# Kernel optimization log

Measured on AMD Instinct MI355X. Metric: run time of the kernel, lower is better.

Reference implementation:

```python
import jax, jax.numpy as jnp
import numpy as np

B, N, C, H, MLP = 4, 1024, 768, 6, 2304  # num_heads = C // 128
D = C // H  # head dim = 128


def setup_inputs() -> dict:
    key = jax.random.key(0)
    ks = iter(jax.random.split(key, 64))
    def nrm(shape, s=0.02):
        return jax.random.normal(next(ks), shape, jnp.float32) * s
    inp = {}
    for nm in ("queries", "change_emb", "imageA_emb", "imageB_emb", "pe"):
        inp[nm] = jax.random.normal(next(ks), (B, N, C), jnp.float32)
    # three Attention modules: self-attn (1), change->ABC cross (2), imageAB->change cross (3)
    for i in (1, 2, 3):
        for p in ("q", "k", "v", "o"):
            inp[f"w{p}{i}"] = nrm((C, C))       # stored [in, out]; y = x @ W + b
            inp[f"b{p}{i}"] = jnp.zeros((C,), jnp.float32)
    for i in (1, 2, 3):
        inp[f"ln{i}_w"] = jnp.ones((C,), jnp.float32)
        inp[f"ln{i}_b"] = jnp.zeros((C,), jnp.float32)
    inp["mlp_w1"] = nrm((C, MLP)); inp["mlp_b1"] = jnp.zeros((MLP,), jnp.float32)
    inp["mlp_w2"] = nrm((MLP, C)); inp["mlp_b2"] = jnp.zeros((C,), jnp.float32)
    inp["flag_a"] = nrm((C,)); inp["flag_b"] = nrm((C,)); inp["flag_c"] = nrm((C,))
    return inp


def _ln(x, w, b, eps=1e-5):
    m = jnp.mean(x, -1, keepdims=True)
    v = jnp.var(x, -1, keepdims=True)
    return (x - m) * jax.lax.rsqrt(v + eps) * w + b


def _mha(q, k, v, wq, bq, wk, bk, wv, bv, wo, bo):
    b, nq, _ = q.shape
    qh = (q @ wq + bq).reshape(b, nq, H, D)
    kh = (k @ wk + bk).reshape(b, k.shape[1], H, D)
    vh = (v @ wv + bv).reshape(b, v.shape[1], H, D)
    scores = jnp.einsum('bqhd,bkhd->bhqk', qh, kh) / np.float32(np.sqrt(D))
    attn = jax.nn.softmax(scores, axis=-1)
    out = jnp.einsum('bhqk,bkhd->bqhd', attn, vh).reshape(b, nq, H * D)
    return out @ wo + bo


def reference(queries, change_emb, imageA_emb, imageB_emb, pe,
              wq1, bq1, wk1, bk1, wv1, bv1, wo1, bo1,
              wq2, bq2, wk2, bk2, wv2, bv2, wo2, bo2,
              wq3, bq3, wk3, bk3, wv3, bv3, wo3, bo3,
              ln1_w, ln1_b, ln2_w, ln2_b, ln3_w, ln3_b,
              mlp_w1, mlp_b1, mlp_w2, mlp_b2,
              flag_a, flag_b, flag_c):
    # --- self attention on change queries (skip_first_layer_add=False) ---
    q0 = queries + change_emb
    a = _mha(q0 + pe, q0 + pe, q0, wq1, bq1, wk1, bk1, wv1, bv1, wo1, bo1)
    q1 = _ln(q0 + a, ln1_w, ln1_b)
    # --- cross attention: change -> [imageA, imageB, change] ---
    qf = q1 + pe + flag_c
    k2 = jnp.concatenate((imageA_emb + pe + flag_a,
                          imageB_emb + pe + flag_b,
                          q1 + pe + flag_c), axis=1)
    v2 = jnp.concatenate((imageA_emb, imageB_emb, q1), axis=1)
    a = _mha(qf, k2, v2, wq2, bq2, wk2, bk2, wv2, bv2, wo2, bo2)
    q2 = _ln(q1 + a, ln2_w, ln2_b)
    # --- MLP (exact GELU, as nn.GELU default) ---
    mlp_out = jax.nn.gelu(q2 @ mlp_w1 + mlp_b1, approximate=False) @ mlp_w2 + mlp_b2
    q3 = _ln(q2 + mlp_out, ln3_w, ln3_b)
    change_out = q3
    # --- cross attention: [imageA; imageB] -> [image; change], batched along dim 0 ---
    qa = imageA_emb + pe + flag_a
    qb = imageB_emb + pe + flag_b
    ka = jnp.concatenate((imageA_emb + pe + flag_a, q3 + pe + flag_c), axis=1)
    kb = jnp.concatenate((imageB_emb + pe + flag_b, q3 + pe + flag_c), axis=1)
    va = jnp.concatenate((imageA_emb, q3), axis=1)
    vb = jnp.concatenate((imageB_emb, q3), axis=1)
    q = jnp.concatenate((qa, qb), axis=0)   # [2B, N, C]
    k = jnp.concatenate((ka, kb), axis=0)   # [2B, 2N, C]
    v = jnp.concatenate((va, vb), axis=0)
    a = _mha(q, k, v, wq3, bq3, wk3, bk3, wv3, bv3, wo3, bo3)
    q = q + a
    image_A_refined, image_B_refined = jnp.split(q, 2, axis=0)
    return (image_A_refined, image_B_refined, change_out)
```

## Files before the change

kernel.cpp:

```cpp
#include <hip/hip_runtime.h>
#include <hip/hip_bf16.h>
#include <math.h>

typedef short bf16x8 __attribute__((ext_vector_type(8)));
typedef float f32x4 __attribute__((ext_vector_type(4)));
using bf16_t = __hip_bfloat16;

#define DEV static __device__ __forceinline__

DEV unsigned short f2bu(float x) {
  bf16_t h = __float2bfloat16(x);
  unsigned short u;
  __builtin_memcpy(&u, &h, 2);
  return u;
}
DEV void st4(bf16_t* p, float a, float b, float c, float d) {
  ushort4 u;
  u.x = f2bu(a); u.y = f2bu(b); u.z = f2bu(c); u.w = f2bu(d);
  *reinterpret_cast<ushort4*>(p) = u;
}

DEV int xcd_swz(int orig, int tot) {
  int q = tot >> 3, r = tot & 7;
  int xcd = orig & 7, pos = orig >> 3;
  int base = xcd < r ? xcd * (q + 1) : r * (q + 1) + (xcd - r) * q;
  return base + pos;
}

DEV void async_copy16(const bf16_t* g, bf16_t* lds) {
  __builtin_amdgcn_global_load_lds(
      (const __attribute__((address_space(1))) unsigned int*)g,
      (__attribute__((address_space(3))) unsigned int*)lds, 16, 0, 0);
}

struct WPack {
  const float* s[13];
  bf16_t* d[13];
  float scale[13];
};

__global__ __launch_bounds__(256) void k_wt13(WPack pk) {
  __shared__ float tile[32][33];
  int z = blockIdx.z;
  const float* W = pk.s[z];
  bf16_t* WT = pk.d[z];
  float scale = pk.scale[z];
  int i0 = blockIdx.x * 32;
  int o0 = blockIdx.y * 32;
  int tx = threadIdx.x & 31, ty = threadIdx.x >> 5;
  for (int r = ty; r < 32; r += 8)
    tile[r][tx] = W[(size_t)(i0 + r) * 768 + (o0 + tx)];
  __syncthreads();
  for (int r = ty; r < 32; r += 8)
    WT[(size_t)(o0 + r) * 768 + (i0 + tx)] = __float2bfloat16(tile[tx][r] * scale);
}

__global__ __launch_bounds__(256) void k_wt(const float* __restrict__ W, bf16_t* __restrict__ WT,
                                            int in_dim, int out_dim) {
  __shared__ float tile[32][33];
  int i0 = blockIdx.x * 32;
  int o0 = blockIdx.y * 32;
  int tx = threadIdx.x & 31, ty = threadIdx.x >> 5;
  for (int r = ty; r < 32; r += 8)
    tile[r][tx] = W[(size_t)(i0 + r) * out_dim + (o0 + tx)];
  __syncthreads();
  for (int r = ty; r < 32; r += 8)
    WT[(size_t)(o0 + r) * in_dim + (i0 + tx)] = __float2bfloat16(tile[tx][r]);
}

__global__ __launch_bounds__(256) void k_bcat(const float* __restrict__ s0, const float* __restrict__ s1,
                                              const float* __restrict__ s2, float a0,
                                              float* __restrict__ out, int nseg) {
  int i = blockIdx.x * 256 + threadIdx.x;
  if (i >= nseg * 768) return;
  int seg = i / 768, c = i - seg * 768;
  const float* s = seg == 0 ? s0 : (seg == 1 ? s1 : s2);
  out[i] = s[c] * (seg == 0 ? a0 : 1.0f);
}

__global__ __launch_bounds__(256) void k_prep1(const float4* __restrict__ q, const float4* __restrict__ ce,
                                               const float4* __restrict__ pe,
                                               bf16_t* __restrict__ qpe_b, bf16_t* __restrict__ q0_b, int n4) {
  int i = blockIdx.x * 256 + threadIdx.x;
  if (i >= n4) return;
  float4 a = q[i], b = ce[i], p = pe[i];
  float sx = a.x + b.x, sy = a.y + b.y, sz = a.z + b.z, sw = a.w + b.w;
  st4(q0_b + 4 * (size_t)i, sx, sy, sz, sw);
  st4(qpe_b + 4 * (size_t)i, sx + p.x, sy + p.y, sz + p.z, sw + p.w);
}

__global__ __launch_bounds__(256) void k_buildqq(const float* __restrict__ imA, const float* __restrict__ imB,
                                                 const float* __restrict__ pe, const float* __restrict__ fa,
                                                 const float* __restrict__ fb, bf16_t* __restrict__ qq,
                                                 bf16_t* __restrict__ imAB) {
  int idx = blockIdx.x * 256 + threadIdx.x;
  int c4 = idx % 192; int rem = idx / 192;
  int n = rem & 1023; int bb = rem >> 10;
  int b = bb & 3, isB = bb >> 2;
  int c = c4 * 4;
  size_t tok = (size_t)(b * 1024 + n) * 768 + c;
  float4 s = *(const float4*)((isB ? imB : imA) + tok);
  float4 p = *(const float4*)(pe + tok);
  float4 f = *(const float4*)((isB ? fb : fa) + c);
  size_t o = (size_t)rem * 768 + c;
  st4(imAB + o, s.x, s.y, s.z, s.w);
  st4(qq + o, s.x + p.x + f.x, s.y + p.y + f.y, s.z + p.z + f.z, s.w + p.w + f.w);
}

struct FArgs {
  const bf16_t* Q; bf16_t* O;
  const bf16_t* Kp[3]; const bf16_t* Vp[3];
  int badd[3], bmask[3];
  int ldq, ldk;
  long qStrideB, oStrideB;
};

template<int NSEG>
__global__ __launch_bounds__(256, 3) void k_flash(FArgs fa) {
  const int z = blockIdx.y; const int b = z / 6, h = z % 6;
  const bf16_t* Qb = fa.Q + (size_t)b * fa.qStrideB + h * 128;
  bf16_t* Ob = fa.O + (size_t)b * fa.oStrideB + h * 128;
  const int q0 = blockIdx.x * 64;
  const int tid = threadIdx.x, lane = tid & 63, w = tid >> 6;
  const int g = lane >> 4, c = lane & 15;

  __shared__ bf16_t Ks[64][136];
  __shared__ bf16_t Vs[128][72];
  __shared__ bf16_t Ps[64][72];

  bf16x8 qf[4];
#pragma unroll
  for (int kk = 0; kk < 4; kk++)
    qf[kk] = *reinterpret_cast<const bf16x8*>(
        &Qb[(size_t)(q0 + w * 16 + c) * fa.ldq + kk * 32 + g * 8]);

  f32x4 oa[8];
  float m[4], l[4];
#pragma unroll
  for (int d = 0; d < 8; d++) { f32x4 zz = {0.f, 0.f, 0.f, 0.f}; oa[d] = zz; }
#pragma unroll
  for (int r = 0; r < 4; r++) { m[r] = -1.0e30f; l[r] = 0.f; }

  const int kr_ = tid >> 4, kc_ = (tid & 15) * 8;
  const int vr_ = tid >> 3, vc_ = (tid & 7) * 8;
  const int ldk = fa.ldk;

#pragma unroll
  for (int s = 0; s < NSEG; ++s) {
    const int bi = fa.badd[s] + (b & fa.bmask[s]);
    const bf16_t* Kb = fa.Kp[s] + (size_t)bi * 1024 * ldk + h * 128;
    const bf16_t* Vb = fa.Vp[s] + (size_t)(bi * 6 + h) * 128 * 1024;
    for (int t = 0; t < 16; ++t) {
      const int k0 = t << 6;
#pragma unroll
      for (int p = 0; p < 4; p++)
        *reinterpret_cast<uint4*>(&Ks[p * 16 + kr_][kc_]) =
            *reinterpret_cast<const uint4*>(&Kb[(size_t)(k0 + p * 16 + kr_) * ldk + kc_]);
#pragma unroll
      for (int p = 0; p < 4; p++)
        *reinterpret_cast<uint4*>(&Vs[p * 32 + vr_][vc_]) =
            *reinterpret_cast<const uint4*>(&Vb[(size_t)(p * 32 + vr_) * 1024 + k0 + vc_]);
      __syncthreads();

      f32x4 sx[4];
#pragma unroll
      for (int j = 0; j < 4; j++) { f32x4 zz = {0.f, 0.f, 0.f, 0.f}; sx[j] = zz; }
      __builtin_amdgcn_s_setprio(1);
#pragma unroll
      for (int kk = 0; kk < 4; kk++)
#pragma unroll
        for (int j = 0; j < 4; j++) {
          bf16x8 kf = *reinterpret_cast<const bf16x8*>(&Ks[j * 16 + c][kk * 32 + g * 8]);
          sx[j] = __builtin_amdgcn_mfma_f32_16x16x32_bf16(qf[kk], kf, sx[j], 0, 0, 0);
        }
      __builtin_amdgcn_s_setprio(0);

      float tl[4];
#pragma unroll
      for (int r = 0; r < 4; r++)
        tl[r] = fmaxf(fmaxf(sx[0][r], sx[1][r]), fmaxf(sx[2][r], sx[3][r]));
      float ex = fmaxf(fmaxf(tl[0] - m[0], tl[1] - m[1]), fmaxf(tl[2] - m[2], tl[3] - m[3]));
      if (__any(ex > 8.0f)) {
#pragma unroll
        for (int r = 0; r < 4; r++) {
          float tv = tl[r];
          tv = fmaxf(tv, __shfl_xor(tv, 1));
          tv = fmaxf(tv, __shfl_xor(tv, 2));
          tv = fmaxf(tv, __shfl_xor(tv, 4));
          tv = fmaxf(tv, __shfl_xor(tv, 8));
          float mn = fmaxf(m[r], tv);
          float f = exp2f(m[r] - mn);
          m[r] = mn;
          l[r] *= f;
#pragma unroll
          for (int d = 0; d < 8; d++) oa[d][r] *= f;
        }
      }
#pragma unroll
      for (int j = 0; j < 4; j++)
#pragma unroll
        for (int r = 0; r < 4; r++) {
          float p = exp2f(sx[j][r] - m[r]);
          l[r] += p;
          Ps[w * 16 + g * 4 + r][j * 16 + c] = __float2bfloat16(p);
        }

      __builtin_amdgcn_s_setprio(1);
#pragma unroll
      for (int kk = 0; kk < 2; kk++) {
        bf16x8 pf = *reinterpret_cast<const bf16x8*>(&Ps[w * 16 + c][kk * 32 + g * 8]);
#pragma unroll
        for (int d = 0; d < 8; d++) {
          bf16x8 vf = *reinterpret_cast<const bf16x8*>(&Vs[d * 16 + c][kk * 32 + g * 8]);
          oa[d] = __builtin_amdgcn_mfma_f32_16x16x32_bf16(pf, vf, oa[d], 0, 0, 0);
        }
      }
      __builtin_amdgcn_s_setprio(0);
      __syncthreads();
    }
  }

  float inv[4];
#pragma unroll
  for (int r = 0; r < 4; r++) {
    float t2 = l[r];
    t2 += __shfl_xor(t2, 1);
    t2 += __shfl_xor(t2, 2);
    t2 += __shfl_xor(t2, 4);
    t2 += __shfl_xor(t2, 8);
    inv[r] = 1.0f / t2;
  }
#pragma unroll
  for (int d = 0; d < 8; d++) {
    int col = d * 16 + c;
#pragma unroll
    for (int r = 0; r < 4; r++) {
      int row = q0 + w * 16 + g * 4 + r;
      Ob[(size_t)row * 768 + col] = __float2bfloat16(oa[d][r] * inv[r]);
    }
  }
}

__global__ __launch_bounds__(256) void k_ln(const float* __restrict__ X1, const float* __restrict__ X2,
                                            const float* __restrict__ A,
                                            const float* __restrict__ w, const float* __restrict__ bvec,
                                            float* __restrict__ outf, bf16_t* __restrict__ outb,
                                            const float* __restrict__ pe, const float* __restrict__ flag,
                                            bf16_t* __restrict__ outpf) {
  int row = blockIdx.x, tid = threadIdx.x;
  size_t base = (size_t)row * 768;
  float v0 = X1[base + tid] + A[base + tid];
  float v1 = X1[base + tid + 256] + A[base + tid + 256];
  float v2 = X1[base + tid + 512] + A[base + tid + 512];
  if (X2) {
    v0 += X2[base + tid]; v1 += X2[base + tid + 256]; v2 += X2[base + tid + 512];
  }
  float s = v0 + v1 + v2;
  for (int o = 32; o; o >>= 1) s += __shfl_xor(s, o);
  __shared__ float sm[8];
  int wv = tid >> 6, ln = tid & 63;
  if (ln == 0) sm[wv] = s;
  __syncthreads();
  s = sm[0] + sm[1] + sm[2] + sm[3];
  float mean = s * (1.0f / 768.0f);
  float d0 = v0 - mean, d1 = v1 - mean, d2 = v2 - mean;
  float ss = d0 * d0 + d1 * d1 + d2 * d2;
  for (int o = 32; o; o >>= 1) ss += __shfl_xor(ss, o);
  if (ln == 0) sm[4 + wv] = ss;
  __syncthreads();
  ss = sm[4] + sm[5] + sm[6] + sm[7];
  float rstd = rsqrtf(ss * (1.0f / 768.0f) + 1e-5f);
  float o0 = d0 * rstd * w[tid] + bvec[tid];
  float o1 = d1 * rstd * w[tid + 256] + bvec[tid + 256];
  float o2 = d2 * rstd * w[tid + 512] + bvec[tid + 512];
  outf[base + tid] = o0; outf[base + tid + 256] = o1; outf[base + tid + 512] = o2;
  if (outb) {
    outb[base + tid] = __float2bfloat16(o0);
    outb[base + tid + 256] = __float2bfloat16(o1);
    outb[base + tid + 512] = __float2bfloat16(o2);
  }
  if (outpf) {
    outpf[base + tid] = __float2bfloat16(o0 + pe[base + tid] + flag[tid]);
    outpf[base + tid + 256] = __float2bfloat16(o1 + pe[base + tid + 256] + flag[tid + 256]);
    outpf[base + tid + 512] = __float2bfloat16(o2 + pe[base + tid + 512] + flag[tid + 512]);
  }
}

struct GArgs {
  const bf16_t* X; const bf16_t* Wt; const float* bias;
  void* O0; void* O1; void* O2;
  const bf16_t* resid;
  int K, ldx, ldw, ldo, vNk, mode;
};
struct GPack {
  GArgs a[7];
  int cum[7];
  int nx[7];
  int tot;
};

__global__ __launch_bounds__(256, 2) void k_gemmN(GPack pk) {
  GArgs a; int gbase, nx;
  int sidx = xcd_swz(blockIdx.x, pk.tot);
  {
    int idx = sidx;
    if (idx < pk.cum[0])      { a = pk.a[0]; gbase = 0;          nx = pk.nx[0]; }
    else if (idx < pk.cum[1]) { a = pk.a[1]; gbase = pk.cum[0];  nx = pk.nx[1]; }
    else if (idx < pk.cum[2]) { a = pk.a[2]; gbase = pk.cum[1];  nx = pk.nx[2]; }
    else if (idx < pk.cum[3]) { a = pk.a[3]; gbase = pk.cum[2];  nx = pk.nx[3]; }
    else if (idx < pk.cum[4]) { a = pk.a[4]; gbase = pk.cum[3];  nx = pk.nx[4]; }
    else if (idx < pk.cum[5]) { a = pk.a[5]; gbase = pk.cum[4];  nx = pk.nx[5]; }
    else                      { a = pk.a[6]; gbase = pk.cum[5];  nx = pk.nx[6]; }
  }
  int idx = sidx - gbase;
  const int brow = (idx / nx) * 128;
  const int bcol = (idx % nx) * 128;

  __shared__ bf16_t As[128 * 32];
  __shared__ bf16_t Bs[128 * 32];

  const int tid = threadIdx.x;
  const int lane = tid & 63;
  const int wave = tid >> 6;
  const int wr = wave >> 1;
  const int wc = wave & 1;

  f32x4 acc[4][4];
#pragma unroll
  for (int i = 0; i < 4; i++)
#pragma unroll
    for (int j = 0; j < 4; j++) {
      f32x4 zz = {0.f, 0.f, 0.f, 0.f};
      acc[i][j] = zz;
    }

  const int sr = lane >> 2;
  const int sc = (lane & 3) * 8;
  const int lrow = lane & 15;
  const int kch = (lane >> 4) * 8;

  const int nK = a.K >> 5;
  for (int kk = 0; kk < nK; ++kk) {
    const int k0 = kk << 5;
#pragma unroll
    for (int q = 0; q < 2; q++) {
      const int rows = wave * 32 + q * 16;
      async_copy16(a.X + (size_t)(brow + rows + sr) * a.ldx + k0 + sc, As + rows * 32);
      async_copy16(a.Wt + (size_t)(bcol + rows + sr) * a.ldw + k0 + sc, Bs + rows * 32);
    }
    __syncthreads();

    bf16x8 afr[4], bfr[4];
#pragma unroll
    for (int i = 0; i < 4; i++)
      afr[i] = *reinterpret_cast<const bf16x8*>(&As[(wr * 64 + i * 16 + lrow) * 32 + kch]);
#pragma unroll
    for (int j = 0; j < 4; j++)
      bfr[j] = *reinterpret_cast<const bf16x8*>(&Bs[(wc * 64 + j * 16 + lrow) * 32 + kch]);
#pragma unroll
    for (int i = 0; i < 4; i++)
#pragma unroll
      for (int j = 0; j < 4; j++)
        acc[i][j] = __builtin_amdgcn_mfma_f32_16x16x32_bf16(afr[i], bfr[j], acc[i][j], 0, 0, 0);
    __syncthreads();
  }

  const int lcol = lane & 15;
  const int lrow4 = (lane >> 4) * 4;

  int seg = 0;
  if (a.O1) seg = bcol / 768;
  void* ob = seg == 0 ? a.O0 : (seg == 1 ? a.O1 : a.O2);
  const int cofs = seg * 768;

  if (a.mode == 2) {
    const int bi = brow / a.vNk;
    const int n0 = brow - bi * a.vNk;
#pragma unroll
    for (int i = 0; i < 4; i++) {
      int rloc = n0 + wr * 64 + i * 16 + lrow4;
#pragma unroll
      for (int j = 0; j < 4; j++) {
        int colf = bcol + wc * 64 + j * 16 + lcol;
        int col = colf - cofs;
        int hh = col >> 7, dd = col & 127;
        float bv = a.bias[colf];
        ushort4 u;
        u.x = f2bu(acc[i][j][0] + bv);
        u.y = f2bu(acc[i][j][1] + bv);
        u.z = f2bu(acc[i][j][2] + bv);
        u.w = f2bu(acc[i][j][3] + bv);
        bf16_t* dst = reinterpret_cast<bf16_t*>(ob) +
                      ((size_t)(bi * 6 + hh) * 128 + dd) * (size_t)a.vNk + rloc;
        *reinterpret_cast<ushort4*>(dst) = u;
      }
    }
  } else if (a.mode == 3) {
#pragma unroll
    for (int i = 0; i < 4; i++) {
      int row0 = brow + wr * 64 + i * 16 + lrow4;
#pragma unroll
      for (int j = 0; j < 4; j++) {
        int col = bcol + wc * 64 + j * 16 + lcol;
        float bv = a.bias[col];
#pragma unroll
        for (int r = 0; r < 4; r++) {
          size_t idx2 = (size_t)(row0 + r) * a.ldo + col;
          float rv = __bfloat162float(a.resid[(size_t)(row0 + r) * 768 + col]);
          reinterpret_cast<float*>(a.O0)[idx2] = acc[i][j][r] + bv + rv;
        }
      }
    }
  } else {
#pragma unroll
    for (int i = 0; i < 4; i++) {
      int row0 = brow + wr * 64 + i * 16 + lrow4;
#pragma unroll
      for (int j = 0; j < 4; j++) {
        int colf = bcol + wc * 64 + j * 16 + lcol;
        int col = colf - cofs;
        float bv = a.bias[colf];
#pragma unroll
        for (int r = 0; r < 4; r++)
          reinterpret_cast<bf16_t*>(ob)[(size_t)(row0 + r) * a.ldo + col] =
              __float2bfloat16(acc[i][j][r] + bv);
      }
    }
  }
}

static inline void packN(hipStream_t st, const GArgs* as, const int* Ms, const int* Ns, int n) {
  GPack pk;
  int tot = 0;
  for (int i = 0; i < 7; ++i) {
    int j = i < n ? i : n - 1;
    pk.a[i] = as[j];
    pk.nx[i] = Ns[j] / 128;
    if (i < n) tot += (Ns[j] / 128) * (Ms[j] / 128);
    pk.cum[i] = tot;
  }
  pk.tot = tot;
  k_gemmN<<<dim3(tot), 256, 0, st>>>(pk);
}

template<int OUTBF, int GELU>
__global__ __launch_bounds__(256, 2) void k_gemm(
    const bf16_t* __restrict__ X, const bf16_t* __restrict__ Wt,
    const float* __restrict__ bias, void* __restrict__ Out,
    int M, int Nout, int K, int ldx, int ldw, int ldo, float alpha) {
  int tot = gridDim.x * gridDim.y;
  int lin = blockIdx.y * gridDim.x + blockIdx.x;
  int sidx = xcd_swz(lin, tot);
  const int brow = (sidx / gridDim.x) * 128;
  const int bcol = (sidx % gridDim.x) * 128;

  __shared__ bf16_t As[128 * 32];
  __shared__ bf16_t Bs[128 * 32];

  const int tid = threadIdx.x;
  const int lane = tid & 63;
  const int wave = tid >> 6;
  const int wr = wave >> 1;
  const int wc = wave & 1;

  f32x4 acc[4][4];
#pragma unroll
  for (int i = 0; i < 4; i++)
#pragma unroll
    for (int j = 0; j < 4; j++) {
      f32x4 zz = {0.f, 0.f, 0.f, 0.f};
      acc[i][j] = zz;
    }

  const int sr = lane >> 2;
  const int sc = (lane & 3) * 8;
  const int lrow = lane & 15;
  const int kch = (lane >> 4) * 8;

  const int nK = K >> 5;
  for (int kk = 0; kk < nK; ++kk) {
    const int k0 = kk << 5;
#pragma unroll
    for (int q = 0; q < 2; q++) {
      const int rows = wave * 32 + q * 16;
      async_copy16(X + (size_t)(brow + rows + sr) * ldx + k0 + sc, As + rows * 32);
      async_copy16(Wt + (size_t)(bcol + rows + sr) * ldw + k0 + sc, Bs + rows * 32);
    }
    __syncthreads();

    bf16x8 afr[4], bfr[4];
#pragma unroll
    for (int i = 0; i < 4; i++)
      afr[i] = *reinterpret_cast<const bf16x8*>(&As[(wr * 64 + i * 16 + lrow) * 32 + kch]);
#pragma unroll
    for (int j = 0; j < 4; j++)
      bfr[j] = *reinterpret_cast<const bf16x8*>(&Bs[(wc * 64 + j * 16 + lrow) * 32 + kch]);
#pragma unroll
    for (int i = 0; i < 4; i++)
#pragma unroll
      for (int j = 0; j < 4; j++)
        acc[i][j] = __builtin_amdgcn_mfma_f32_16x16x32_bf16(afr[i], bfr[j], acc[i][j], 0, 0, 0);
    __syncthreads();
  }

  const int lcol = lane & 15;
  const int lrow4 = (lane >> 4) * 4;

#pragma unroll
  for (int i = 0; i < 4; i++) {
    int row0 = brow + wr * 64 + i * 16 + lrow4;
#pragma unroll
    for (int j = 0; j < 4; j++) {
      int col = bcol + wc * 64 + j * 16 + lcol;
      float bv = bias ? bias[col] : 0.0f;
#pragma unroll
      for (int r = 0; r < 4; r++) {
        float v = (acc[i][j][r] + bv) * alpha;
        if (GELU) v = 0.5f * v * (1.0f + erff(v * 0.70710678118f));
        size_t idx = (size_t)(row0 + r) * ldo + col;
        if (OUTBF) reinterpret_cast<bf16_t*>(Out)[idx] = __float2bfloat16(v);
        else reinterpret_cast<float*>(Out)[idx] = v;
      }
    }
  }
}

static inline void gemm(hipStream_t st, const bf16_t* X, const bf16_t* Wt, const float* bias,
                        void* out, int outBf, int gelu, int M, int N, int K,
                        int ldx, int ldw, int ldo, float alpha = 1.0f) {
  dim3 g(N / 128, M / 128), blk(256);
  if (outBf) {
    if (gelu) k_gemm<1, 1><<<g, blk, 0, st>>>(X, Wt, bias, out, M, N, K, ldx, ldw, ldo, alpha);
    else      k_gemm<1, 0><<<g, blk, 0, st>>>(X, Wt, bias, out, M, N, K, ldx, ldw, ldo, alpha);
  } else      k_gemm<0, 0><<<g, blk, 0, st>>>(X, Wt, bias, out, M, N, K, ldx, ldw, ldo, alpha);
}

extern "C" void kernel_launch(void* const* d_in, const int* in_sizes, int n_in,
                              void* d_out, int out_size, void* d_ws, size_t ws_size,
                              hipStream_t stream) {
  (void)in_sizes; (void)n_in; (void)out_size; (void)ws_size;
  constexpr int B = 4, N = 1024, C = 768, Hh = 6, MLPD = 2304;
  constexpr size_t BNC = (size_t)B * N * C;
  constexpr size_t NC  = (size_t)N * C;
  const float qalpha = 0.08838834764831845f * 1.4426950408889634f;

  const float* queries = (const float*)d_in[0];
  const float* change  = (const float*)d_in[1];
  const float* imA     = (const float*)d_in[2];
  const float* imB     = (const float*)d_in[3];
  const float* pe      = (const float*)d_in[4];
  const float* bq1 = (const float*)d_in[6];  const float* bk1 = (const float*)d_in[8];
  const float* bv1 = (const float*)d_in[10]; const float* bo1 = (const float*)d_in[12];
  const float* bq2 = (const float*)d_in[14]; const float* bk2 = (const float*)d_in[16];
  const float* bv2 = (const float*)d_in[18]; const float* bo2 = (const float*)d_in[20];
  const float* bq3 = (const float*)d_in[22]; const float* bk3 = (const float*)d_in[24];
  const float* bv3 = (const float*)d_in[26]; const float* bo3 = (const float*)d_in[28];
  const float* ln1w = (const float*)d_in[29]; const float* ln1b = (const float*)d_in[30];
  const float* ln2w = (const float*)d_in[31]; const float* ln2b = (const float*)d_in[32];
  const float* ln3w = (const float*)d_in[33]; const float* ln3b = (const float*)d_in[34];
  const float* mb1 = (const float*)d_in[36]; const float* mb2 = (const float*)d_in[38];
  const float* fa = (const float*)d_in[39];
  const float* fb = (const float*)d_in[40];
  const float* fc = (const float*)d_in[41];

  char* base = (char*)d_ws;
  size_t off = 0;
  auto alloc = [&](size_t bytes) -> void* {
    void* p = base + off;
    off += (bytes + 255) & ~(size_t)255;
    return p;
  };

  bf16_t* WT[12]; bf16_t* WT5b; bf16_t* WTm1; bf16_t* WTm2;
  WT[0] = (bf16_t*)alloc((size_t)768 * 768 * 2);
  WT[1] = (bf16_t*)alloc((size_t)768 * 768 * 2);
  WT[2] = (bf16_t*)alloc((size_t)768 * 768 * 2);
  WT[3] = (bf16_t*)alloc((size_t)768 * 768 * 2);
  WT[8] = (bf16_t*)alloc((size_t)768 * 768 * 2);
  WT[5] = (bf16_t*)alloc((size_t)768 * 768 * 2);
  WT[9] = (bf16_t*)alloc((size_t)768 * 768 * 2);
  WT[6] = (bf16_t*)alloc((size_t)768 * 768 * 2);
  WT[10] = (bf16_t*)alloc((size_t)768 * 768 * 2);
  WT[4] = (bf16_t*)alloc((size_t)768 * 768 * 2);
  WT5b  = (bf16_t*)alloc((size_t)768 * 768 * 2);
  WT[7] = (bf16_t*)alloc((size_t)768 * 768 * 2);
  WT[11] = (bf16_t*)alloc((size_t)768 * 768 * 2);
  WTm1 = (bf16_t*)alloc((size_t)768 * 2304 * 2);
  WTm2 = (bf16_t*)alloc((size_t)2304 * 768 * 2);
  float* bqk1  = (float*)alloc(1536 * 4);
  float* bKm   = (float*)alloc(2304 * 4);
  float* bVm   = (float*)alloc(1536 * 4);
  float* bQ2K2 = (float*)alloc(1536 * 4);
  float*  q1  = (float*)alloc(BNC * 4);
  float*  q2  = (float*)alloc(BNC * 4);
  bf16_t* q2b = (bf16_t*)alloc(BNC * 2);
  bf16_t* q1b = (bf16_t*)alloc(BNC * 2);
  bf16_t* qf  = (bf16_t*)alloc(BNC * 2);
  bf16_t* qq   = (bf16_t*)alloc(2 * BNC * 2);
  bf16_t* Q3h  = (bf16_t*)alloc(2 * BNC * 2);
  bf16_t* K2i  = (bf16_t*)alloc(2 * BNC * 2);
  bf16_t* vT2i = (bf16_t*)alloc(2 * BNC * 2);
  bf16_t* K3i  = (bf16_t*)alloc(2 * BNC * 2);
  bf16_t* vT3i = (bf16_t*)alloc(2 * BNC * 2);
  const size_t arena = off;

  float* dof = (float*)d_out;
  float* chg = dof + 2 * BNC;

  {
    WPack pk;
    const int widx[12] = {5, 7, 9, 11, 13, 15, 17, 19, 21, 23, 25, 27};
    for (int i = 0; i < 12; i++) {
      pk.s[i] = (const float*)d_in[widx[i]];
      pk.d[i] = WT[i];
      pk.scale[i] = (i == 0 || i == 4 || i == 8) ? qalpha : 1.0f;
    }
    pk.s[12] = (const float*)d_in[15]; pk.d[12] = WT5b; pk.scale[12] = 1.0f;
    k_wt13<<<dim3(24, 24, 13), 256, 0, stream>>>(pk);
  }
  k_wt<<<dim3(24, 72), 256, 0, stream>>>((const float*)d_in[35], WTm1, 768, 2304);
  k_wt<<<dim3(72, 24), 256, 0, stream>>>((const float*)d_in[37], WTm2, 2304, 768);
  k_bcat<<<dim3(6), 256, 0, stream>>>(bq1, bk1, nullptr, qalpha, bqk1, 2);
  k_bcat<<<dim3(9), 256, 0, stream>>>(bq3, bk2, bk3, qalpha, bKm, 3);
  k_bcat<<<dim3(6), 256, 0, stream>>>(bv2, bv3, nullptr, 1.0f, bVm, 2);
  k_bcat<<<dim3(6), 256, 0, stream>>>(bq2, bk2, nullptr, qalpha, bQ2K2, 2);

  off = arena;
  bf16_t* qpe_b = (bf16_t*)alloc(BNC * 2);
  bf16_t* q0_b  = (bf16_t*)alloc(BNC * 2);
  bf16_t* imAB  = (bf16_t*)alloc(2 * BNC * 2);
  bf16_t* QKh   = (bf16_t*)alloc((size_t)B * N * 1536 * 2);
  bf16_t* vT1   = (bf16_t*)alloc(BNC * 2);
  bf16_t* attC  = (bf16_t*)alloc(BNC * 2);
  float*  a1    = dof;

  k_prep1<<<dim3((int)(BNC / 4 / 256)), 256, 0, stream>>>(
      (const float4*)queries, (const float4*)change, (const float4*)pe, qpe_b, q0_b, (int)(BNC / 4));
  k_buildqq<<<dim3((int)(2 * BNC / 4 / 256)), 256, 0, stream>>>(imA, imB, pe, fa, fb, qq, imAB);
  {
    GArgs as[4] = {
      {qpe_b, WT[0], bqk1, QKh,  nullptr, nullptr, nullptr, C, C, C, 1536, 0,    1},
      {q0_b,  WT[2], bv1,  vT1,  nullptr, nullptr, nullptr, C, C, C, 0,    1024, 2},
      {qq,    WT[8], bKm,  Q3h,  K2i,     K3i,     nullptr, C, C, C, 768,  0,    1},
      {imAB,  WT[6], bVm,  vT2i, vT3i,    nullptr, nullptr, C, C, C, 0,    1024, 2},
    };
    int Ms[4] = {B * N, B * N, 2 * B * N, 2 * B * N};
    int Ns[4] = {1536, C, 2304, 1536};
    packN(stream, as, Ms, Ns, 4);
  }
  {
    FArgs f1 = {QKh, attC, {QKh + 768, QKh + 768, QKh + 768}, {vT1, vT1, vT1},
                {0, 0, 0}, {7, 7, 7}, 1536, 1536, (long)N * 1536, (long)NC};
    k_flash<1><<<dim3(16, B * Hh), 256, 0, stream>>>(f1);
  }
  gemm(stream, attC, WT[3], bo1, a1, 0, 0, B * N, C, C, C, C, C);
  k_ln<<<dim3(B * N), 256, 0, stream>>>(queries, change, a1, ln1w, ln1b, q1, q1b, pe, fc, qf);

  off = arena;
  bf16_t* Q2h   = (bf16_t*)alloc(BNC * 2);
  bf16_t* K2c   = (bf16_t*)alloc(BNC * 2);
  bf16_t* vT2c  = (bf16_t*)alloc(BNC * 2);
  bf16_t* attC2 = (bf16_t*)alloc(BNC * 2);
  float*  a2    = dof;

  {
    GArgs as[2] = {
      {qf,  WT[4], bQ2K2, Q2h,  K2c,    nullptr, nullptr, C, C, C, 768,  0,    1},
      {q1b, WT[6], bv2,   vT2c, nullptr, nullptr, nullptr, C, C, C, 0,    1024, 2},
    };
    int Ms[2] = {B * N, B * N};
    int Ns[2] = {1536, C};
    packN(stream, as, Ms, Ns, 2);
  }
  {
    FArgs f2 = {Q2h, attC2, {K2i, K2i, K2c}, {vT2i, vT2i, vT2c},
                {0, 4, 0}, {3, 3, 3}, C, C, (long)NC, (long)NC};
    k_flash<3><<<dim3(16, B * Hh), 256, 0, stream>>>(f2);
  }
  gemm(stream, attC2, WT[7], bo2, a2, 0, 0, B * N, C, C, C, C, C);
  k_ln<<<dim3(B * N), 256, 0, stream>>>(q1, (const float*)nullptr, a2, ln2w, ln2b, q2, q2b,
                                        (const float*)nullptr, (const float*)nullptr, (bf16_t*)nullptr);

  off = arena;
  bf16_t* h1 = (bf16_t*)alloc((size_t)B * N * MLPD * 2);
  float*  a3 = dof;
  gemm(stream, q2b, WTm1, mb1, h1, 1, 1, B * N, MLPD, C, C, C, MLPD);
  gemm(stream, h1, WTm2, mb2, a3, 0, 0, B * N, C, MLPD, MLPD, MLPD, C);

  off = arena;
  bf16_t* cf    = (bf16_t*)alloc(BNC * 2);
  bf16_t* chgb  = (bf16_t*)alloc(BNC * 2);
  bf16_t* K3c   = (bf16_t*)alloc(BNC * 2);
  bf16_t* vT3c  = (bf16_t*)alloc(BNC * 2);
  bf16_t* attC3 = (bf16_t*)alloc(2 * BNC * 2);

  k_ln<<<dim3(B * N), 256, 0, stream>>>(q2, (const float*)nullptr, a3, ln3w, ln3b, chg, chgb,
                                        pe, fc, cf);
  {
    GArgs as[2] = {
      {cf,   WT[9],  bk3, K3c,  nullptr, nullptr, nullptr, C, C, C, 768,  0,    1},
      {chgb, WT[10], bv3, vT3c, nullptr, nullptr, nullptr, C, C, C, 0,    1024, 2},
    };
    int Ms[2] = {B * N, B * N};
    int Ns[2] = {C, C};
    packN(stream, as, Ms, Ns, 2);
  }
  {
    FArgs f3 = {Q3h, attC3, {K3i, K3c, K3c}, {vT3i, vT3c, vT3c},
                {0, 0, 0}, {7, 3, 3}, C, C, (long)NC, (long)NC};
    k_flash<2><<<dim3(16, 2 * B * Hh), 256, 0, stream>>>(f3);
  }
  {
    GArgs as[1] = {{attC3, WT[11], bo3, dof, nullptr, nullptr, qq, C, C, C, C, 0, 3}};
    int Ms[1] = {2 * B * N};
    int Ns[1] = {C};
    packN(stream, as, Ms, Ns, 1);
  }
}
```

Before: 630.2 us.

## Hoist image-key segment of final cross-attention into the early self-attention launch

The final cross-attention's first segment (image keys and values, which depend only on the inputs) is computed early, fused into the same launch as the first self-attention. It writes unnormalized fp32 partial outputs plus running max and sum to scratch buffers. The final flash kernel then loads that state and processes only the change-token segment. The intent is to fill the GPU better in the small 24-block-row self-attention launch and shorten the critical path of the last attention. In exchange it adds fp32 scratch traffic for the partial output and more register pressure in the resume path.

```diff
diff --git a/kernel.cpp b/kernel.cpp
--- a/kernel.cpp
+++ b/kernel.cpp
@@ -115,18 +115,19 @@
   long qStrideB, oStrideB;
 };
 
-template<int NSEG>
-__global__ __launch_bounds__(256, 3) void k_flash(FArgs fa) {
-  const int z = blockIdx.y; const int b = z / 6, h = z % 6;
+struct SMem {
+  bf16_t Ks[64][136];
+  bf16_t Vs[128][72];
+  bf16_t Ps[64][72];
+};
+
+template<int NSEG, int OMODE>
+DEV void flash_body(const FArgs& fa, int z, int q0, SMem& sm,
+                    float* __restrict__ Of, float* __restrict__ Mv, float* __restrict__ Lv) {
+  const int b = z / 6, h = z % 6;
   const bf16_t* Qb = fa.Q + (size_t)b * fa.qStrideB + h * 128;
-  bf16_t* Ob = fa.O + (size_t)b * fa.oStrideB + h * 128;
-  const int q0 = blockIdx.x * 64;
   const int tid = threadIdx.x, lane = tid & 63, w = tid >> 6;
   const int g = lane >> 4, c = lane & 15;
-
-  __shared__ bf16_t Ks[64][136];
-  __shared__ bf16_t Vs[128][72];
-  __shared__ bf16_t Ps[64][72];
 
   bf16x8 qf[4];
 #pragma unroll
@@ -136,10 +137,23 @@
 
   f32x4 oa[8];
   float m[4], l[4];
-#pragma unroll
-  for (int d = 0; d < 8; d++) { f32x4 zz = {0.f, 0.f, 0.f, 0.f}; oa[d] = zz; }
-#pragma unroll
-  for (int r = 0; r < 4; r++) { m[r] = -1.0e30f; l[r] = 0.f; }
+  if (OMODE == 2) {
+#pragma unroll
+    for (int r = 0; r < 4; r++) {
+      int row = b * 1024 + q0 + w * 16 + g * 4 + r;
+      m[r] = Mv[row * 6 + h];
+      float lv = Lv[row * 6 + h];
+      l[r] = (c == 0 && g == 0) ? lv : 0.f;
+#pragma unroll
+      for (int d = 0; d < 8; d++)
+        oa[d][r] = Of[(size_t)row * 768 + h * 128 + d * 16 + c];
+    }
+  } else {
+#pragma unroll
+    for (int d = 0; d < 8; d++) { f32x4 zz = {0.f, 0.f, 0.f, 0.f}; oa[d] = zz; }
+#pragma unroll
+    for (int r = 0; r < 4; r++) { m[r] = -1.0e30f; l[r] = 0.f; }
+  }
 
   const int kr_ = tid >> 4, kc_ = (tid & 15) * 8;
   const int vr_ = tid >> 3, vc_ = (tid & 7) * 8;
@@ -154,11 +168,11 @@
       const int k0 = t << 6;
 #pragma unroll
       for (int p = 0; p < 4; p++)
-        *reinterpret_cast<uint4*>(&Ks[p * 16 + kr_][kc_]) =
+        *reinterpret_cast<uint4*>(&sm.Ks[p * 16 + kr_][kc_]) =
             *reinterpret_cast<const uint4*>(&Kb[(size_t)(k0 + p * 16 + kr_) * ldk + kc_]);
 #pragma unroll
       for (int p = 0; p < 4; p++)
-        *reinterpret_cast<uint4*>(&Vs[p * 32 + vr_][vc_]) =
+        *reinterpret_cast<uint4*>(&sm.Vs[p * 32 + vr_][vc_]) =
             *reinterpret_cast<const uint4*>(&Vb[(size_t)(p * 32 + vr_) * 1024 + k0 + vc_]);
       __syncthreads();
 
@@ -170,7 +184,7 @@
       for (int kk = 0; kk < 4; kk++)
 #pragma unroll
         for (int j = 0; j < 4; j++) {
-          bf16x8 kf = *reinterpret_cast<const bf16x8*>(&Ks[j * 16 + c][kk * 32 + g * 8]);
+          bf16x8 kf = *reinterpret_cast<const bf16x8*>(&sm.Ks[j * 16 + c][kk * 32 + g * 8]);
           sx[j] = __builtin_amdgcn_mfma_f32_16x16x32_bf16(qf[kk], kf, sx[j], 0, 0, 0);
         }
       __builtin_amdgcn_s_setprio(0);
@@ -202,16 +216,16 @@
         for (int r = 0; r < 4; r++) {
           float p = exp2f(sx[j][r] - m[r]);
           l[r] += p;
-          Ps[w * 16 + g * 4 + r][j * 16 + c] = __float2bfloat16(p);
+          sm.Ps[w * 16 + g * 4 + r][j * 16 + c] = __float2bfloat16(p);
         }
 
       __builtin_amdgcn_s_setprio(1);
 #pragma unroll
       for (int kk = 0; kk < 2; kk++) {
-        bf16x8 pf = *reinterpret_cast<const bf16x8*>(&Ps[w * 16 + c][kk * 32 + g * 8]);
+        bf16x8 pf = *reinterpret_cast<const bf16x8*>(&sm.Ps[w * 16 + c][kk * 32 + g * 8]);
 #pragma unroll
         for (int d = 0; d < 8; d++) {
-          bf16x8 vf = *reinterpret_cast<const bf16x8*>(&Vs[d * 16 + c][kk * 32 + g * 8]);
+          bf16x8 vf = *reinterpret_cast<const bf16x8*>(&sm.Vs[d * 16 + c][kk * 32 + g * 8]);
           oa[d] = __builtin_amdgcn_mfma_f32_16x16x32_bf16(pf, vf, oa[d], 0, 0, 0);
         }
       }
@@ -220,25 +234,70 @@
     }
   }
 
-  float inv[4];
-#pragma unroll
-  for (int r = 0; r < 4; r++) {
-    float t2 = l[r];
-    t2 += __shfl_xor(t2, 1);
-    t2 += __shfl_xor(t2, 2);
-    t2 += __shfl_xor(t2, 4);
-    t2 += __shfl_xor(t2, 8);
-    inv[r] = 1.0f / t2;
-  }
-#pragma unroll
-  for (int d = 0; d < 8; d++) {
-    int col = d * 16 + c;
+  if (OMODE == 1) {
+    float lr[4];
 #pragma unroll
     for (int r = 0; r < 4; r++) {
-      int row = q0 + w * 16 + g * 4 + r;
-      Ob[(size_t)row * 768 + col] = __float2bfloat16(oa[d][r] * inv[r]);
-    }
-  }
+      float t2 = l[r];
+      t2 += __shfl_xor(t2, 1);
+      t2 += __shfl_xor(t2, 2);
+      t2 += __shfl_xor(t2, 4);
+      t2 += __shfl_xor(t2, 8);
+      lr[r] = t2;
+    }
+#pragma unroll
+    for (int r = 0; r < 4; r++) {
+      int row = b * 1024 + q0 + w * 16 + g * 4 + r;
+#pragma unroll
+      for (int d = 0; d < 8; d++)
+        Of[(size_t)row * 768 + h * 128 + d * 16 + c] = oa[d][r];
+      if (c == 0 && g == 0) {
+        Mv[row * 6 + h] = m[r];
+        Lv[row * 6 + h] = lr[r];
+      }
+    }
+  } else {
+    bf16_t* Ob = fa.O + (size_t)b * fa.oStrideB + h * 128;
+    float inv[4];
+#pragma unroll
+    for (int r = 0; r < 4; r++) {
+      float t2 = l[r];
+      t2 += __shfl_xor(t2, 1);
+      t2 += __shfl_xor(t2, 2);
+      t2 += __shfl_xor(t2, 4);
+      t2 += __shfl_xor(t2, 8);
+      inv[r] = 1.0f / t2;
+    }
+#pragma unroll
+    for (int d = 0; d < 8; d++) {
+      int col = d * 16 + c;
+#pragma unroll
+      for (int r = 0; r < 4; r++) {
+        int row = q0 + w * 16 + g * 4 + r;
+        Ob[(size_t)row * 768 + col] = __float2bfloat16(oa[d][r] * inv[r]);
+      }
+    }
+  }
+}
+
+template<int NSEG>
+__global__ __launch_bounds__(256, 3) void k_flash(FArgs fa) {
+  __shared__ SMem sm;
+  flash_body<NSEG, 0>(fa, blockIdx.y, blockIdx.x * 64, sm, nullptr, nullptr, nullptr);
+}
+
+__global__ __launch_bounds__(256, 3) void k_flash_pair(FArgs f1a, FArgs f3a, int ny0,
+                                                       float* Of, float* Mv, float* Lv) {
+  __shared__ SMem sm;
+  if ((int)blockIdx.y < ny0)
+    flash_body<1, 0>(f1a, blockIdx.y, blockIdx.x * 64, sm, nullptr, nullptr, nullptr);
+  else
+    flash_body<1, 1>(f3a, blockIdx.y - ny0, blockIdx.x * 64, sm, Of, Mv, Lv);
+}
+
+__global__ __launch_bounds__(256, 3) void k_flash_fin(FArgs fa, float* Of, float* Mv, float* Lv) {
+  __shared__ SMem sm;
+  flash_body<1, 2>(fa, blockIdx.y, blockIdx.x * 64, sm, Of, Mv, Lv);
 }
 
 __global__ __launch_bounds__(256) void k_ln(const float* __restrict__ X1, const float* __restrict__ X2,
@@ -602,6 +661,9 @@
   bf16_t* vT2i = (bf16_t*)alloc(2 * BNC * 2);
   bf16_t* K3i  = (bf16_t*)alloc(2 * BNC * 2);
   bf16_t* vT3i = (bf16_t*)alloc(2 * BNC * 2);
+  float*  Of3  = (float*)alloc(2 * BNC * 4);
+  float*  Mv3  = (float*)alloc((size_t)2 * B * N * 6 * 4);
+  float*  Lv3  = (float*)alloc((size_t)2 * B * N * 6 * 4);
   const size_t arena = off;
 
   float* dof = (float*)d_out;
@@ -649,9 +711,11 @@
     packN(stream, as, Ms, Ns, 4);
   }
   {
-    FArgs f1 = {QKh, attC, {QKh + 768, QKh + 768, QKh + 768}, {vT1, vT1, vT1},
-                {0, 0, 0}, {7, 7, 7}, 1536, 1536, (long)N * 1536, (long)NC};
-    k_flash<1><<<dim3(16, B * Hh), 256, 0, stream>>>(f1);
+    FArgs f1a = {QKh, attC, {QKh + 768, QKh + 768, QKh + 768}, {vT1, vT1, vT1},
+                 {0, 0, 0}, {7, 7, 7}, 1536, 1536, (long)N * 1536, (long)NC};
+    FArgs f3a = {Q3h, nullptr, {K3i, K3i, K3i}, {vT3i, vT3i, vT3i},
+                 {0, 0, 0}, {7, 7, 7}, C, C, (long)NC, (long)NC};
+    k_flash_pair<<<dim3(16, 24 + 48), 256, 0, stream>>>(f1a, f3a, 24, Of3, Mv3, Lv3);
   }
   gemm(stream, attC, WT[3], bo1, a1, 0, 0, B * N, C, C, C, C, C);
   k_ln<<<dim3(B * N), 256, 0, stream>>>(queries, change, a1, ln1w, ln1b, q1, q1b, pe, fc, qf);
@@ -706,9 +770,9 @@
     packN(stream, as, Ms, Ns, 2);
   }
   {
-    FArgs f3 = {Q3h, attC3, {K3i, K3c, K3c}, {vT3i, vT3c, vT3c},
-                {0, 0, 0}, {7, 3, 3}, C, C, (long)NC, (long)NC};
-    k_flash<2><<<dim3(16, 2 * B * Hh), 256, 0, stream>>>(f3);
+    FArgs f3b = {Q3h, attC3, {K3c, K3c, K3c}, {vT3c, vT3c, vT3c},
+                 {0, 0, 0}, {3, 3, 3}, C, C, (long)NC, (long)NC};
+    k_flash_fin<<<dim3(16, 2 * B * Hh), 256, 0, stream>>>(f3b, Of3, Mv3, Lv3);
   }
   {
     GArgs as[1] = {{attC3, WT[11], bo3, dof, nullptr, nullptr, qq, C, C, C, C, 0, 3}};
```

Result: no change. 638.7 us (+1.3%).
